# Kernel tuning notes

Measured on AMD Instinct MI355X. Metric: run time of the kernel, lower is better.

## Reference

```python
import jax, jax.numpy as jnp
import numpy as np

A = 9            # n_anchor = len(ratios)*len(anchor_scales)
STRIDE = 16      # feat_stride
IMG_H = 1024
IMG_W = 1024
MIN_SIZE = 16.0  # min_size * scale (scale=1.0)
PRE_NMS = 2000
POST_NMS = 300
NMS_THRESH = 0.7


def _anchor_base():
    base = 16.0
    ratios = np.array([0.5, 1.0, 2.0])
    scales = np.array([8.0, 16.0, 32.0])
    ab = np.zeros((A, 4), np.float32)
    px = py = base / 2.0
    for i, r in enumerate(ratios):
        for j, s in enumerate(scales):
            h = base * s * np.sqrt(r)
            w = base * s * np.sqrt(1.0 / r)
            ab[i * 3 + j] = [py - h / 2, px - w / 2, py + h / 2, px + w / 2]
    return ab


def _all_anchors(hh, ww):
    ab = _anchor_base()
    sy = np.arange(0, hh * STRIDE, STRIDE)
    sx = np.arange(0, ww * STRIDE, STRIDE)
    sx, sy = np.meshgrid(sx, sy)
    shift = np.stack((sy.ravel(), sx.ravel(), sy.ravel(), sx.ravel()), axis=1)
    anc = (ab[None, :, :] + shift[:, None, :]).reshape(-1, 4).astype(np.float32)
    return jnp.asarray(anc)  # [hh*ww*A, 4] in (y1,x1,y2,x2)


def _conv(x, w, b, pad):
    y = jax.lax.conv_general_dilated(
        x, w, (1, 1), [(pad, pad), (pad, pad)],
        dimension_numbers=('NCHW', 'OIHW', 'NCHW'))
    return y + b[None, :, None, None]


def _loc2bbox(anc, loc):
    h = anc[:, 2] - anc[:, 0]
    w = anc[:, 3] - anc[:, 1]
    cy = anc[:, 0] + 0.5 * h
    cx = anc[:, 1] + 0.5 * w
    dy, dx, dh, dw = loc[:, 0], loc[:, 1], loc[:, 2], loc[:, 3]
    cy2 = dy * h + cy
    cx2 = dx * w + cx
    h2 = jnp.exp(dh) * h
    w2 = jnp.exp(dw) * w
    return jnp.stack([cy2 - 0.5 * h2, cx2 - 0.5 * w2,
                      cy2 + 0.5 * h2, cx2 + 0.5 * w2], axis=1)


def _iou_matrix(b):
    tl = jnp.maximum(b[:, None, :2], b[None, :, :2])
    br = jnp.minimum(b[:, None, 2:], b[None, :, 2:])
    inter = jnp.prod(jnp.clip(br - tl, 0.0), axis=-1)
    area = jnp.prod(b[:, 2:] - b[:, :2], axis=-1)
    return inter / (area[:, None] + area[None, :] - inter + 1e-9)


def _propose(fg, loc, anc):
    # fg: [K*A] foreground scores, loc: [K*A, 4] deltas
    boxes = _loc2bbox(anc, loc)
    boxes = jnp.stack([jnp.clip(boxes[:, 0], 0.0, IMG_H),
                       jnp.clip(boxes[:, 1], 0.0, IMG_W),
                       jnp.clip(boxes[:, 2], 0.0, IMG_H),
                       jnp.clip(boxes[:, 3], 0.0, IMG_W)], axis=1)
    hs = boxes[:, 2] - boxes[:, 0]
    ws = boxes[:, 3] - boxes[:, 1]
    valid = (hs >= MIN_SIZE) & (ws >= MIN_SIZE)
    fg = jnp.where(valid, fg, -jnp.inf)
    sc, idx = jax.lax.top_k(fg, PRE_NMS)          # sorted desc by score
    b = boxes[idx]                                 # [PRE_NMS, 4]
    iou = jax.lax.stop_gradient(_iou_matrix(b))    # indices/masks are constants
    keep0 = sc > -jnp.inf
    ar = jnp.arange(PRE_NMS)

    def body(i, keep):
        sup = (iou[i] > NMS_THRESH) & keep[i] & (ar > i)
        return keep & ~sup

    keep = jax.lax.fori_loop(0, PRE_NMS, body, keep0)
    order = jnp.where(keep, ar, PRE_NMS)
    sel = jnp.sort(order)[:POST_NMS]
    ok = sel < PRE_NMS
    sel = jnp.minimum(sel, PRE_NMS - 1)
    rois = jnp.where(ok[:, None], b[sel], 0.0)     # [POST_NMS, 4], zero-padded
    return rois


def setup_inputs() -> dict:
    key = jax.random.key(0)
    ks = jax.random.split(key, 4)
    x = jax.random.normal(ks[0], (8, 512, 64, 64), dtype=jnp.float32)
    conv1_w = jax.random.normal(ks[1], (512, 512, 3, 3), dtype=jnp.float32) * 0.01
    conv1_b = jnp.zeros((512,), jnp.float32)
    score_w = jax.random.normal(ks[2], (2 * A, 512, 1, 1), dtype=jnp.float32) * 0.01
    score_b = jnp.zeros((2 * A,), jnp.float32)
    loc_w = jax.random.normal(ks[3], (4 * A, 512, 1, 1), dtype=jnp.float32) * 0.01
    loc_b = jnp.zeros((4 * A,), jnp.float32)
    return {'x': x, 'conv1_w': conv1_w, 'conv1_b': conv1_b,
            'score_w': score_w, 'score_b': score_b,
            'loc_w': loc_w, 'loc_b': loc_b}


def reference(x, conv1_w, conv1_b, score_w, score_b, loc_w, loc_b):
    n, _, hh, ww = x.shape
    h = jax.nn.relu(_conv(x, conv1_w, conv1_b, 1))
    loc = _conv(h, loc_w, loc_b, 0)                # [n, 4A, hh, ww]
    score = _conv(h, score_w, score_b, 0)          # [n, 2A, hh, ww]
    rpn_locs = loc.transpose(0, 2, 3, 1).reshape(n, -1, 4)      # [n, hh*ww*A, 4]
    rpn_scores = score.transpose(0, 2, 3, 1).reshape(n, -1, 2)  # [n, hh*ww*A, 2]
    fg = jax.nn.softmax(rpn_scores.reshape(n, hh, ww, A, 2), axis=-1)[..., 1]
    fg = fg.reshape(n, -1)                         # [n, hh*ww*A]
    anc = _all_anchors(hh, ww)
    rois = jax.vmap(lambda f, l: _propose(f, l, anc))(fg, rpn_locs)  # [n, POST_NMS, 4]
    roi_indices = jnp.repeat(jnp.arange(n, dtype=jnp.int32), POST_NMS)
    return rpn_locs, rpn_scores, rois.reshape(-1, 4), roi_indices, anc
```

## Files before the change

### kernel.cpp

```cpp
#include <hip/hip_runtime.h>
#include <math.h>
#include <stdint.h>

#define NB 8
#define CIN 512
#define HW 4096
#define ANUM 9
#define NANC 36864
#define PRE 2000
#define POST 300

#define OUT_LOCS   0
#define OUT_SCORES 1179648
#define OUT_ROIS   1769472
#define OUT_RIDX   1779072
#define OUT_ANC    1781472

typedef _Float16 half8 __attribute__((ext_vector_type(8)));
typedef float f32x4 __attribute__((ext_vector_type(4)));

#define WSCALE 256.0f
#define LSCALE 4096.0f
#define INV_WS (1.0f / 256.0f)
#define INV_LS (1.0f / 4096.0f)
#define XS_STRIDE 40

__global__ void anchor_kernel(float* __restrict__ out) {
  int i = blockIdx.x * 256 + threadIdx.x;
  if (i >= NANC) return;
  int s = i / 9, a = i - s * 9;
  int y = s >> 6, x = s & 63;
  int ri = a / 3, si = a - ri * 3;
  double r = (ri == 0) ? 0.5 : (ri == 1 ? 1.0 : 2.0);
  double sc = (si == 0) ? 8.0 : (si == 1 ? 16.0 : 32.0);
  double hh = 16.0 * sc * sqrt(r);
  double ww = 16.0 * sc * sqrt(1.0 / r);
  float a0 = (float)(8.0 - hh * 0.5);
  float a1 = (float)(8.0 - ww * 0.5);
  float a2 = (float)(8.0 + hh * 0.5);
  float a3 = (float)(8.0 + ww * 0.5);
  float sy = (float)(y * 16), sx = (float)(x * 16);
  out[OUT_ANC + i * 4 + 0] = a0 + sy;
  out[OUT_ANC + i * 4 + 1] = a1 + sx;
  out[OUT_ANC + i * 4 + 2] = a2 + sy;
  out[OUT_ANC + i * 4 + 3] = a3 + sx;
}

__global__ void wprep_kernel(const float* __restrict__ w, _Float16* __restrict__ Bf) {
  int i = blockIdx.x * 256 + threadIdx.x;
  int j = i & 7;
  int l = (i >> 3) & 63;
  int limb = (i >> 9) & 1;
  int ob = (i >> 10) & 31;
  int icb = (i >> 15) & 15;
  int tap = i >> 19;
  int ic = icb * 32 + ((l >> 4) << 3) + j;
  int oc = (ob << 4) + (l & 15);
  float v = w[((size_t)oc * CIN + ic) * 9 + tap] * WSCALE;
  _Float16 hi = (_Float16)v;
  Bf[i] = limb ? (_Float16)((v - (float)hi) * LSCALE) : hi;
}

__global__ __launch_bounds__(256) void conv3_mfma(
    const float* __restrict__ x, const _Float16* __restrict__ Bf,
    const float* __restrict__ bias, float* __restrict__ h) {
  __shared__ _Float16 xhi[2][108 * XS_STRIDE];
  __shared__ _Float16 xlo[2][108 * XS_STRIDE];
  int blk = blockIdx.x;
  int ntblk = blk & 3;
  int mb = blk >> 2;
  int img = mb >> 6;
  int t = mb & 63;
  int ty0 = (t >> 2) * 4, tx0 = (t & 3) * 16;
  int tid = threadIdx.x;
  int wv = tid >> 6, lane = tid & 63;
  int col = lane & 15, quad = lane >> 4;

  f32x4 acc0[4][2], accC[4][2];
#pragma unroll
  for (int g = 0; g < 4; ++g)
#pragma unroll
    for (int nt = 0; nt < 2; ++nt) {
      acc0[g][nt] = (f32x4){0.f, 0.f, 0.f, 0.f};
      accC[g][nt] = (f32x4){0.f, 0.f, 0.f, 0.f};
    }

  int goffs[4];
  int laddr[4];
#pragma unroll
  for (int s = 0; s < 4; ++s) {
    int l = tid + (s << 8);
    bool act = (l < 864);
    int icg = l / 108;
    int pos = l - icg * 108;
    int py = pos / 18, px = pos - py * 18;
    int gy = ty0 - 1 + py, gx = tx0 - 1 + px;
    bool inb = act && ((unsigned)gy < 64u) && ((unsigned)gx < 64u);
    goffs[s] = inb ? ((icg << 14) + (gy << 6) + gx) : -1;
    laddr[s] = act ? (pos * XS_STRIDE + (icg << 2)) : -1;
  }

  const float* xn = x + ((size_t)img << 21);
  const half8* B8 = (const half8*)Bf;
  const half8* Bq = B8 + (((size_t)(ntblk * 8 + wv * 2)) << 7) + lane;
  int abase = col * XS_STRIDE + quad * 8;

  typedef _Float16 h4 __attribute__((ext_vector_type(4)));

  {
    const float* xb = xn;
#pragma unroll
    for (int s = 0; s < 4; ++s) {
      if (laddr[s] >= 0) {
        float v0 = 0.f, v1 = 0.f, v2 = 0.f, v3 = 0.f;
        if (goffs[s] >= 0) {
          const float* p = xb + goffs[s];
          v0 = p[0]; v1 = p[HW]; v2 = p[2 * HW]; v3 = p[3 * HW];
        }
        _Float16 h0 = (_Float16)v0, h1 = (_Float16)v1;
        _Float16 h2 = (_Float16)v2, h3 = (_Float16)v3;
        _Float16 e0 = (_Float16)((v0 - (float)h0) * LSCALE);
        _Float16 e1 = (_Float16)((v1 - (float)h1) * LSCALE);
        _Float16 e2 = (_Float16)((v2 - (float)h2) * LSCALE);
        _Float16 e3 = (_Float16)((v3 - (float)h3) * LSCALE);
        *(h4*)(xhi[0] + laddr[s]) = (h4){h0, h1, h2, h3};
        *(h4*)(xlo[0] + laddr[s]) = (h4){e0, e1, e2, e3};
      }
    }
  }
  __syncthreads();

#pragma unroll 1
  for (int icb = 0; icb < 16; ++icb) {
    int cur = icb & 1;
    float pv0[4], pv1[4], pv2[4], pv3[4];
    const int nxt = icb + 1;
    if (nxt < 16) {
      const float* xb = xn + ((size_t)nxt << 17);
#pragma unroll
      for (int s = 0; s < 4; ++s) {
        pv0[s] = 0.f; pv1[s] = 0.f; pv2[s] = 0.f; pv3[s] = 0.f;
        if (goffs[s] >= 0) {
          const float* p = xb + goffs[s];
          pv0[s] = p[0]; pv1[s] = p[HW]; pv2[s] = p[2 * HW]; pv3[s] = p[3 * HW];
        }
      }
    }
    const _Float16* xh = xhi[cur];
    const _Float16* xl = xlo[cur];
    __builtin_amdgcn_s_setprio(1);
#pragma unroll
    for (int ky = 0; ky < 3; ++ky) {
#pragma unroll
      for (int kx = 0; kx < 3; ++kx) {
        int tap = ky * 3 + kx;
        size_t boff = ((size_t)(tap * 16 + icb)) << 12;
        half8 Bh0 = Bq[boff];
        half8 Bl0 = Bq[boff + 64];
        half8 Bh1 = Bq[boff + 128];
        half8 Bl1 = Bq[boff + 192];
        int toff = (ky * 18 + kx) * XS_STRIDE + abase;
#pragma unroll
        for (int g = 0; g < 4; ++g) {
          int off = toff + g * (18 * XS_STRIDE);
          half8 Ah = *(const half8*)(xh + off);
          half8 Al = *(const half8*)(xl + off);
          acc0[g][0] = __builtin_amdgcn_mfma_f32_16x16x32_f16(Ah, Bh0, acc0[g][0], 0, 0, 0);
          accC[g][0] = __builtin_amdgcn_mfma_f32_16x16x32_f16(Ah, Bl0, accC[g][0], 0, 0, 0);
          accC[g][0] = __builtin_amdgcn_mfma_f32_16x16x32_f16(Al, Bh0, accC[g][0], 0, 0, 0);
          acc0[g][1] = __builtin_amdgcn_mfma_f32_16x16x32_f16(Ah, Bh1, acc0[g][1], 0, 0, 0);
          accC[g][1] = __builtin_amdgcn_mfma_f32_16x16x32_f16(Ah, Bl1, accC[g][1], 0, 0, 0);
          accC[g][1] = __builtin_amdgcn_mfma_f32_16x16x32_f16(Al, Bh1, accC[g][1], 0, 0, 0);
        }
      }
    }
    __builtin_amdgcn_s_setprio(0);
    if (nxt < 16) {
      _Float16* wh = xhi[cur ^ 1];
      _Float16* wl = xlo[cur ^ 1];
#pragma unroll
      for (int s = 0; s < 4; ++s) {
        if (laddr[s] >= 0) {
          float v0 = pv0[s], v1 = pv1[s], v2 = pv2[s], v3 = pv3[s];
          _Float16 h0 = (_Float16)v0, h1 = (_Float16)v1;
          _Float16 h2 = (_Float16)v2, h3 = (_Float16)v3;
          _Float16 e0 = (_Float16)((v0 - (float)h0) * LSCALE);
          _Float16 e1 = (_Float16)((v1 - (float)h1) * LSCALE);
          _Float16 e2 = (_Float16)((v2 - (float)h2) * LSCALE);
          _Float16 e3 = (_Float16)((v3 - (float)h3) * LSCALE);
          *(h4*)(wh + laddr[s]) = (h4){h0, h1, h2, h3};
          *(h4*)(wl + laddr[s]) = (h4){e0, e1, e2, e3};
        }
      }
    }
    __syncthreads();
  }
#pragma unroll
  for (int g = 0; g < 4; ++g) {
#pragma unroll
    for (int nt = 0; nt < 2; ++nt) {
      int oc = (ntblk << 7) + (wv << 5) + (nt << 4) + col;
      float bv = bias[oc];
      int gy = ty0 + g;
      int gx0 = tx0 + (quad << 2);
      f32x4 a0 = acc0[g][nt];
      f32x4 ac = accC[g][nt];
      float4 o;
      o.x = fmaf(ac.x, INV_LS, a0.x) * INV_WS + bv; o.x = o.x > 0.f ? o.x : 0.f;
      o.y = fmaf(ac.y, INV_LS, a0.y) * INV_WS + bv; o.y = o.y > 0.f ? o.y : 0.f;
      o.z = fmaf(ac.z, INV_LS, a0.z) * INV_WS + bv; o.z = o.z > 0.f ? o.z : 0.f;
      o.w = fmaf(ac.w, INV_LS, a0.w) * INV_WS + bv; o.w = o.w > 0.f ? o.w : 0.f;
      *(float4*)(h + ((size_t)img * CIN + oc) * HW + (gy << 6) + gx0) = o;
    }
  }
}

__global__ __launch_bounds__(256) void heads_kernel(
    const float* __restrict__ h, const float* __restrict__ sw,
    const float* __restrict__ sb, const float* __restrict__ lw,
    const float* __restrict__ lb, float* __restrict__ out,
    float* __restrict__ fgm, float* __restrict__ boxes) {
  __shared__ float wlds[2][64][56];
  __shared__ float part[128][56];
  int tid = threadIdx.x;
  int sl = tid >> 7;
  int pl = tid & 127;
  int blk = blockIdx.x;
  int n = blk >> 5;
  int s0 = (blk & 31) * 128;

  float acc[54];
#pragma unroll
  for (int k = 0; k < 54; k++) acc[k] = 0.f;

  for (int cc = 0; cc < 256; cc += 64) {
    for (int l = tid; l < 2 * 64 * 54; l += 256) {
      int slc = l / (64 * 54); int rem = l - slc * 64 * 54;
      int cl = rem / 54; int k = rem - cl * 54;
      int c = slc * 256 + cc + cl;
      wlds[slc][cl][k] = (k < 18) ? sw[k * CIN + c] : lw[(k - 18) * CIN + c];
    }
    __syncthreads();
    int cbase = sl * 256 + cc;
#pragma unroll 4
    for (int cl = 0; cl < 64; ++cl) {
      float hv = h[((size_t)n * CIN + cbase + cl) * HW + s0 + pl];
#pragma unroll
      for (int k = 0; k < 54; ++k) acc[k] = fmaf(hv, wlds[sl][cl][k], acc[k]);
    }
    __syncthreads();
  }
  if (sl == 1) {
#pragma unroll
    for (int k = 0; k < 54; k++) part[pl][k] = acc[k];
  }
  __syncthreads();
  if (sl == 0) {
#pragma unroll
    for (int k = 0; k < 54; k++) acc[k] += part[pl][k];
    int s = s0 + pl;
    int y = s >> 6, xx = s & 63;
    float sc[18], lo[36];
#pragma unroll
    for (int k = 0; k < 18; k++) sc[k] = acc[k] + sb[k];
#pragma unroll
    for (int k = 0; k < 36; k++) lo[k] = acc[18 + k] + lb[k];
    size_t base = (size_t)n * NANC + (size_t)s * 9;
#pragma unroll
    for (int i = 0; i < 36; i++) out[OUT_LOCS + base * 4 + i] = lo[i];
#pragma unroll
    for (int i = 0; i < 18; i++) out[OUT_SCORES + base * 2 + i] = sc[i];
    float syf = (float)(y * 16), sxf = (float)(xx * 16);
#pragma unroll
    for (int a = 0; a < 9; a++) {
      float s0v = sc[a * 2], s1v = sc[a * 2 + 1];
      float m = fmaxf(s0v, s1v);
      float e0 = expf(s0v - m), e1 = expf(s1v - m);
      float fg = e1 / (e0 + e1);
      int ri = a / 3, si = a - ri * 3;
      double r = (ri == 0) ? 0.5 : (ri == 1 ? 1.0 : 2.0);
      double scd = (si == 0) ? 8.0 : (si == 1 ? 16.0 : 32.0);
      double hhd = 16.0 * scd * sqrt(r);
      double wwd = 16.0 * scd * sqrt(1.0 / r);
      float a0 = (float)(8.0 - hhd * 0.5) + syf;
      float a1 = (float)(8.0 - wwd * 0.5) + sxf;
      float a2 = (float)(8.0 + hhd * 0.5) + syf;
      float a3 = (float)(8.0 + wwd * 0.5) + sxf;
      float hA = a2 - a0, wA = a3 - a1;
      float cy = a0 + 0.5f * hA, cx = a1 + 0.5f * wA;
      float dy = lo[a * 4 + 0], dx = lo[a * 4 + 1];
      float dh = lo[a * 4 + 2], dw = lo[a * 4 + 3];
      float cy2 = dy * hA + cy, cx2 = dx * wA + cx;
      float h2 = expf(dh) * hA, w2 = expf(dw) * wA;
      float b0 = cy2 - 0.5f * h2, b1 = cx2 - 0.5f * w2;
      float b2 = cy2 + 0.5f * h2, b3 = cx2 + 0.5f * w2;
      b0 = fminf(fmaxf(b0, 0.f), 1024.f);
      b1 = fminf(fmaxf(b1, 0.f), 1024.f);
      b2 = fminf(fmaxf(b2, 0.f), 1024.f);
      b3 = fminf(fmaxf(b3, 0.f), 1024.f);
      float hs = b2 - b0, wss = b3 - b1;
      bool valid = (hs >= 16.f) && (wss >= 16.f);
      size_t bi = base + a;
      boxes[bi * 4 + 0] = b0; boxes[bi * 4 + 1] = b1;
      boxes[bi * 4 + 2] = b2; boxes[bi * 4 + 3] = b3;
      fgm[bi] = valid ? fg : -__builtin_inff();
    }
  }
}

__device__ __forceinline__ uint32_t ord32(float v) {
  uint32_t s = __float_as_uint(v);
  return (s & 0x80000000u) ? ~s : (s | 0x80000000u);
}

__global__ __launch_bounds__(1024) void select2_kernel(
    const float* __restrict__ fgm, const float* __restrict__ boxes,
    float4* __restrict__ selb, uint8_t* __restrict__ selv) {
  int n = blockIdx.x;
  const float* f = fgm + (size_t)n * NANC;
  __shared__ uint32_t hist[256];
  __shared__ uint32_t segsum[16], segsufE[16];
  __shared__ uint64_t keys[2048];
  __shared__ uint32_t sh_digit, sh_T, scnt;
  int tid = threadIdx.x;
  uint32_t pref = 0;
  uint32_t T = PRE;
  for (int p = 0; p < 4; ++p) {
    int shift = 24 - 8 * p;
    if (tid < 256) hist[tid] = 0;
    __syncthreads();
    for (int i = tid; i < NANC; i += 1024) {
      uint32_t u = ord32(f[i]);
      bool match = (p == 0) || ((u >> (shift + 8)) == (pref >> (shift + 8)));
      if (match) atomicAdd(&hist[(u >> shift) & 255u], 1u);
    }
    __syncthreads();
    if (tid < 16) {
      uint32_t s = 0;
      for (int j = 0; j < 16; ++j) s += hist[tid * 16 + j];
      segsum[tid] = s;
    }
    __syncthreads();
    if (tid == 0) {
      uint32_t run = 0;
      for (int s = 15; s >= 0; --s) { segsufE[s] = run; run += segsum[s]; }
    }
    __syncthreads();
    if (tid < 256) {
      int d = tid, s = d >> 4;
      uint32_t loc = 0;
      for (int j = d; j < (s + 1) * 16; ++j) loc += hist[j];
      uint32_t suf = segsufE[s] + loc;
      uint32_t sufn = suf - hist[d];
      if (suf >= T && sufn < T) { sh_digit = (uint32_t)d; sh_T = T - sufn; }
    }
    __syncthreads();
    pref |= sh_digit << shift;
    T = sh_T;
    __syncthreads();
  }
  if (tid == 0) scnt = 0;
  __syncthreads();
  for (int i = tid; i < NANC; i += 1024) {
    uint32_t u = ord32(f[i]);
    if (u >= pref) {
      uint32_t pos = atomicAdd(&scnt, 1u);
      if (pos < 2048) keys[pos] = ((uint64_t)u << 32) | (uint32_t)(~(uint32_t)i);
    }
  }
  __syncthreads();
  uint32_t sc = scnt > 2048 ? 2048 : scnt;
  for (int i = sc + tid; i < 2048; i += 1024) keys[i] = 0;
  __syncthreads();
  for (int k = 2; k <= 2048; k <<= 1) {
    for (int j = k >> 1; j > 0; j >>= 1) {
      for (int e = tid; e < 2048; e += 1024) {
        int partner = e ^ j;
        if (partner > e) {
          bool up = ((e & k) == 0);
          uint64_t a = keys[e], b = keys[partner];
          if (up ? (a < b) : (a > b)) { keys[e] = b; keys[partner] = a; }
        }
      }
      __syncthreads();
    }
  }
  for (int t2 = tid; t2 < PRE; t2 += 1024) {
    uint64_t key = keys[t2];
    uint32_t idx = ~((uint32_t)(key & 0xFFFFFFFFu));
    const float4* bp = (const float4*)(boxes + ((size_t)n * NANC + idx) * 4);
    selb[(size_t)n * 2048 + t2] = *bp;
    selv[(size_t)n * 2048 + t2] = ((uint32_t)(key >> 32)) > 0x007FFFFFu ? 1 : 0;
  }
}

__global__ __launch_bounds__(256) void nms_mask_kernel(
    const float4* __restrict__ selb, uint64_t* __restrict__ mask) {
  __shared__ float by0[PRE], bx0_[PRE], by1[PRE], bx1_[PRE], bar[PRE];
  int b = blockIdx.x;
  int n = b / 250;
  int i0 = (b % 250) * 8;
  int tid = threadIdx.x;
  for (int j = tid; j < PRE; j += 256) {
    float4 bb = selb[(size_t)n * 2048 + j];
    by0[j] = bb.x; bx0_[j] = bb.y; by1[j] = bb.z; bx1_[j] = bb.w;
    bar[j] = (bb.z - bb.x) * (bb.w - bb.y);
  }
  __syncthreads();
  int i = i0 + (tid >> 5);
  int jw = tid & 31;
  float iy0 = by0[i], ix0 = bx0_[i], iy1 = by1[i], ix1 = bx1_[i], ia = bar[i];
  uint64_t bits = 0;
  int jb = jw * 64;
  for (int tb = 0; tb < 64; ++tb) {
    int tbp = (tb + jw) & 63;
    int j = jb + tbp;
    if (j < PRE && j > i) {
      float ty = fmaxf(iy0, by0[j]);
      float txx = fmaxf(ix0, bx0_[j]);
      float byv = fminf(iy1, by1[j]);
      float bxv = fminf(ix1, bx1_[j]);
      float ih = byv - ty; if (ih < 0.f) ih = 0.f;
      float iw = bxv - txx; if (iw < 0.f) iw = 0.f;
      float inter = ih * iw;
      float iou = inter / (ia + bar[j] - inter + 1e-9f);
      if (iou > 0.7f) bits |= (1ull << tbp);
    }
  }
  mask[((size_t)n * PRE + i) * 32 + jw] = bits;
}

__global__ __launch_bounds__(64) void nms_scan_kernel(
    const uint8_t* __restrict__ selv, const uint64_t* __restrict__ mask,
    const float4* __restrict__ selb, float* __restrict__ out) {
  int n = blockIdx.x;
  int lane = threadIdx.x;
  const uint8_t* sv = selv + (size_t)n * 2048;
  uint64_t kw = 0;
  for (int wblk = 0; wblk < 32; ++wblk) {
    int j = wblk * 64 + lane;
    bool pred = (j < PRE) && (sv[j] != 0);
    uint64_t m = __ballot(pred);
    if (lane == wblk) kw = m;
  }
  const uint64_t* mrow = mask + (size_t)n * PRE * 32;
  int istar = PRE - 1;
  int csf = 0;
  bool done = false;
  for (int i0 = 0; i0 < PRE && !done; i0 += 16) {
    uint64_t rr[16];
#pragma unroll
    for (int tt = 0; tt < 16; ++tt)
      rr[tt] = (lane < 32) ? mrow[(size_t)(i0 + tt) * 32 + lane] : 0;
#pragma unroll
    for (int tt = 0; tt < 16; ++tt) {
      int i = i0 + tt;
      uint64_t w = __shfl(kw, i >> 6);
      if ((w >> (i & 63)) & 1ull) {
        kw &= ~rr[tt];
        csf++;
        if (csf >= POST) { istar = i; done = true; break; }
      }
    }
  }
  int wordi = istar >> 6, biti = istar & 63;
  uint64_t km = (lane < wordi) ? ~0ull
              : (lane == wordi ? ((biti == 63) ? ~0ull : ((1ull << (biti + 1)) - 1ull)) : 0ull);
  uint64_t kwv = (lane < 32) ? (kw & km) : 0ull;
  int pc = __popcll(kwv);
  int pre = pc;
  for (int d = 1; d < 64; d <<= 1) {
    int v = __shfl_up(pre, d);
    if (lane >= d) pre += v;
  }
  int total = __shfl(pre, 63);
  int rank = pre - pc;
  uint64_t bits = kwv;
  while (bits) {
    int bpos = __ffsll((unsigned long long)bits) - 1;
    bits &= bits - 1;
    if (rank < POST) {
      int j = lane * 64 + bpos;
      float4 bx = selb[(size_t)n * 2048 + j];
      size_t o = (size_t)OUT_ROIS + ((size_t)n * POST + rank) * 4;
      out[o + 0] = bx.x; out[o + 1] = bx.y; out[o + 2] = bx.z; out[o + 3] = bx.w;
    }
    rank++;
  }
  int cnt = total > POST ? POST : total;
  for (int r2 = cnt + lane; r2 < POST; r2 += 64) {
    size_t o = (size_t)OUT_ROIS + ((size_t)n * POST + r2) * 4;
    out[o + 0] = 0.f; out[o + 1] = 0.f; out[o + 2] = 0.f; out[o + 3] = 0.f;
  }
  for (int r2 = lane; r2 < POST; r2 += 64)
    out[OUT_RIDX + n * POST + r2] = (float)n;
}

extern "C" void kernel_launch(void* const* d_in, const int* in_sizes, int n_in,
                              void* d_out, int out_size, void* d_ws, size_t ws_size,
                              hipStream_t stream) {
  const float* x   = (const float*)d_in[0];
  const float* c1w = (const float*)d_in[1];
  const float* c1b = (const float*)d_in[2];
  const float* sw  = (const float*)d_in[3];
  const float* sb  = (const float*)d_in[4];
  const float* lw  = (const float*)d_in[5];
  const float* lb  = (const float*)d_in[6];
  float* out = (float*)d_out;
  char* ws = (char*)d_ws;
  float*     hbuf = (float*)(ws);
  float*     fgm  = (float*)(ws + 67108864);
  float*     boxes= (float*)(ws + 68288512);
  _Float16*  Bf   = (_Float16*)(ws + 73007104);
  float4*    selb = (float4*)(ws + 82444288);
  uint8_t*   selv = (uint8_t*)(ws + 82706432);
  uint64_t*  mask = (uint64_t*)(ws + 82722816);

  anchor_kernel<<<144, 256, 0, stream>>>(out);
  wprep_kernel<<<18432, 256, 0, stream>>>(c1w, Bf);
  conv3_mfma<<<2048, 256, 0, stream>>>(x, Bf, c1b, hbuf);
  heads_kernel<<<256, 256, 0, stream>>>(hbuf, sw, sb, lw, lb, out, fgm, boxes);
  select2_kernel<<<8, 1024, 0, stream>>>(fgm, boxes, selb, selv);
  nms_mask_kernel<<<2000, 256, 0, stream>>>(selb, mask);
  nms_scan_kernel<<<8, 64, 0, stream>>>(selv, mask, selb, out);
}
```

Measured before the change: 935.4 us.

## Split conv launch into four chunks and read head weights directly from global

New measurement: 954.3 us. 1.02x slower.

```diff
diff --git a/kernel.cpp b/kernel.cpp
--- a/kernel.cpp
+++ b/kernel.cpp
@@ -63,10 +63,10 @@
 
 __global__ __launch_bounds__(256) void conv3_mfma(
     const float* __restrict__ x, const _Float16* __restrict__ Bf,
-    const float* __restrict__ bias, float* __restrict__ h) {
+    const float* __restrict__ bias, float* __restrict__ h, int blk0) {
   __shared__ _Float16 xhi[2][108 * XS_STRIDE];
   __shared__ _Float16 xlo[2][108 * XS_STRIDE];
-  int blk = blockIdx.x;
+  int blk = blk0 + blockIdx.x;
   int ntblk = blk & 3;
   int mb = blk >> 2;
   int img = mb >> 6;
@@ -220,7 +220,6 @@
     const float* __restrict__ sb, const float* __restrict__ lw,
     const float* __restrict__ lb, float* __restrict__ out,
     float* __restrict__ fgm, float* __restrict__ boxes) {
-  __shared__ float wlds[2][64][56];
   __shared__ float part[128][56];
   int tid = threadIdx.x;
   int sl = tid >> 7;
@@ -233,22 +232,16 @@
 #pragma unroll
   for (int k = 0; k < 54; k++) acc[k] = 0.f;
 
-  for (int cc = 0; cc < 256; cc += 64) {
-    for (int l = tid; l < 2 * 64 * 54; l += 256) {
-      int slc = l / (64 * 54); int rem = l - slc * 64 * 54;
-      int cl = rem / 54; int k = rem - cl * 54;
-      int c = slc * 256 + cc + cl;
-      wlds[slc][cl][k] = (k < 18) ? sw[k * CIN + c] : lw[(k - 18) * CIN + c];
-    }
-    __syncthreads();
-    int cbase = sl * 256 + cc;
-#pragma unroll 4
-    for (int cl = 0; cl < 64; ++cl) {
-      float hv = h[((size_t)n * CIN + cbase + cl) * HW + s0 + pl];
-#pragma unroll
-      for (int k = 0; k < 54; ++k) acc[k] = fmaf(hv, wlds[sl][cl][k], acc[k]);
-    }
-    __syncthreads();
+  int cbase = sl * 256;
+  const float* hp = h + ((size_t)n * CIN + cbase) * HW + s0 + pl;
+#pragma unroll 8
+  for (int cl = 0; cl < 256; ++cl) {
+    float hv = hp[(size_t)cl * HW];
+    int c = cbase + cl;
+#pragma unroll
+    for (int k = 0; k < 18; ++k) acc[k] = fmaf(hv, sw[k * CIN + c], acc[k]);
+#pragma unroll
+    for (int k = 0; k < 36; ++k) acc[18 + k] = fmaf(hv, lw[k * CIN + c], acc[18 + k]);
   }
   if (sl == 1) {
 #pragma unroll
@@ -518,7 +511,10 @@
 
   anchor_kernel<<<144, 256, 0, stream>>>(out);
   wprep_kernel<<<18432, 256, 0, stream>>>(c1w, Bf);
-  conv3_mfma<<<2048, 256, 0, stream>>>(x, Bf, c1b, hbuf);
+  conv3_mfma<<<512, 256, 0, stream>>>(x, Bf, c1b, hbuf, 0);
+  conv3_mfma<<<512, 256, 0, stream>>>(x, Bf, c1b, hbuf, 512);
+  conv3_mfma<<<512, 256, 0, stream>>>(x, Bf, c1b, hbuf, 1024);
+  conv3_mfma<<<512, 256, 0, stream>>>(x, Bf, c1b, hbuf, 1536);
   heads_kernel<<<256, 256, 0, stream>>>(hbuf, sw, sb, lw, lb, out, fgm, boxes);
   select2_kernel<<<8, 1024, 0, stream>>>(fgm, boxes, selb, selv);
   nms_mask_kernel<<<2000, 256, 0, stream>>>(selb, mask);
```
